# Kernel optimization log

Measured on AMD Instinct MI355X. Metric: run time of the kernel, lower is better.

The kernel has to match this reference:

```python
import jax, jax.numpy as jnp
import numpy as np

B, E, C = 1024, 512, 16384
MRG, ALPHA, V, K, LAM, TAU = 0.1, 32.0, 100.0, 1.0, 0.1, 1.5


def _l2norm(x):
    # matches torch l2_norm: divide by sqrt(sum(x^2) + 1e-12) row-wise
    n = jnp.sqrt(jnp.sum(x * x, axis=1) + 1e-12)
    return x / n[:, None]


def setup_inputs() -> dict:
    key = jax.random.key(0)
    k1, k2, k3, k4, k5 = jax.random.split(key, 5)
    inputsBatch = _l2norm(jax.random.normal(k1, (B, E), dtype=jnp.float32))
    targetsBatch = jax.random.randint(k2, (B,), 0, C, dtype=jnp.int32)
    # kaiming_normal fan_out on (C, E): std = sqrt(2 / E)
    proxies = jax.random.normal(k3, (C, E), dtype=jnp.float32) * np.sqrt(2.0 / E).astype(np.float32)
    effectiveNum = jax.random.uniform(k4, (C,), dtype=jnp.float32) * 100.0
    learnedSim = jax.random.uniform(k5, (C,), dtype=jnp.float32)
    return {"inputsBatch": inputsBatch, "targetsBatch": targetsBatch,
            "proxies": proxies, "effectiveNum": effectiveNum, "learnedSim": learnedSim}


def reference(inputsBatch, targetsBatch, proxies, effectiveNum, learnedSim):
    nb_classes = proxies.shape[0]
    P = jax.nn.one_hot(targetsBatch, nb_classes, dtype=inputsBatch.dtype)  # [B, C]
    N = 1.0 - P
    proxy_l2 = _l2norm(proxies)
    cos = inputsBatch @ proxy_l2.T  # [B, C]

    classCnt = P.sum(axis=0)                      # [C]
    present = (classCnt > 0).astype(cos.dtype)

    w_base = 1.0 / (1.0 + jnp.log1p(effectiveNum))
    eta = (1.0 + K * (1.0 - learnedSim)) * w_base + LAM
    outlierSim = learnedSim - eta                 # [C]

    # enableFilter=False: mask at positive positions stays 1, so each present
    # class contributes mean(ones)=1 to pos_weight_sum
    pos_weight_sum = jnp.sum(present)

    # negative-position adaptive reweighting (vectorized over the class loop)
    neg_vals = jnp.where(cos < outlierSim[None, :],
                         (1.0 / jnp.maximum(1.0, effectiveNum))[None, :],
                         1.0)                      # [B, C]
    Ncnt = N.sum(axis=0)
    neg_mean = jnp.sum(N * neg_vals, axis=0) / jnp.maximum(Ncnt, 1.0)
    neg_weight_sum = jnp.sum(jnp.where(Ncnt > 0, neg_mean, 0.0))

    mask = jnp.where(N > 0, neg_vals, 1.0)        # 1 at positive entries

    pos_term = jnp.sum(jnp.log1p(jnp.sum(P * jnp.exp(ALPHA * (MRG - cos) * mask), axis=0)))
    neg_term = jnp.sum(jnp.log1p(jnp.sum(N * jnp.exp(ALPHA * (cos + MRG) * mask), axis=0)))

    return pos_term / pos_weight_sum + neg_term / neg_weight_sum
```

## Files before the change

### kernel.cpp

```cpp
#include <hip/hip_runtime.h>
#include <math.h>

#define B_SZ 1024
#define E_SZ 512
#define C_SZ 16384
#define MRG 0.1f
#define ALPHA 32.0f
#define K_HY 1.0f
#define LAM 0.1f

typedef __bf16 bf16;
typedef bf16 bf16x8 __attribute__((ext_vector_type(8)));
typedef float f32x4 __attribute__((ext_vector_type(4)));

__device__ __forceinline__ void async16(const void* g, void* l) {
    __builtin_amdgcn_global_load_lds(
        (const __attribute__((address_space(1))) void*)g,
        (__attribute__((address_space(3))) void*)l,
        16, 0, 0);
}

__global__ __launch_bounds__(256) void prep(
    const float* __restrict__ effNum, const float* __restrict__ lSim,
    const float* __restrict__ x,
    float* __restrict__ oSim, float* __restrict__ iEff, bf16* __restrict__ Abf,
    float* __restrict__ posExp, float* __restrict__ negExp,
    float* __restrict__ negVals, int* __restrict__ cCnt,
    float* __restrict__ acc4) {
    int c = blockIdx.x * 256 + threadIdx.x;
    float en = effNum[c], ls = lSim[c];
    float wb = 1.0f / (1.0f + log1pf(en));
    float eta = (1.0f + K_HY * (1.0f - ls)) * wb + LAM;
    oSim[c] = ls - eta;
    iEff[c] = 1.0f / fmaxf(1.0f, en);
    posExp[c] = 0.f; negExp[c] = 0.f; negVals[c] = 0.f; cCnt[c] = 0;
    if (c < 8) acc4[c] = 0.f;
    const float* xp = x + (size_t)c * 32;
    bf16* yp = Abf + (size_t)c * 32;
#pragma unroll
    for (int j = 0; j < 4; ++j) {
        float4 v0 = *(const float4*)(xp + j * 8);
        float4 v1 = *(const float4*)(xp + j * 8 + 4);
        bf16x8 o;
        o[0] = (bf16)v0.x; o[1] = (bf16)v0.y; o[2] = (bf16)v0.z; o[3] = (bf16)v0.w;
        o[4] = (bf16)v1.x; o[5] = (bf16)v1.y; o[6] = (bf16)v1.z; o[7] = (bf16)v1.w;
        *(bf16x8*)(yp + j * 8) = o;
    }
}

__global__ __launch_bounds__(256) void proxy_norm(
    const float* __restrict__ proxies, bf16* __restrict__ Pbf,
    const int* __restrict__ tg, int* __restrict__ cCnt) {
    if (blockIdx.x >= 4096) {
        int i = (blockIdx.x - 4096) * 256 + threadIdx.x;
        atomicAdd(&cCnt[tg[i]], 1);
        return;
    }
    int row = (blockIdx.x * 256 + threadIdx.x) >> 6;
    int lane = threadIdx.x & 63;
    const float* pr = proxies + (size_t)row * E_SZ + lane * 8;
    float4 v0 = *(const float4*)pr;
    float4 v1 = *(const float4*)(pr + 4);
    float ss = v0.x * v0.x + v0.y * v0.y + v0.z * v0.z + v0.w * v0.w +
               v1.x * v1.x + v1.y * v1.y + v1.z * v1.z + v1.w * v1.w;
#pragma unroll
    for (int m = 1; m < 64; m <<= 1) ss += __shfl_xor(ss, m);
    float inv = 1.0f / sqrtf(ss + 1e-12f);
    bf16x8 o;
    o[0] = (bf16)(v0.x * inv); o[1] = (bf16)(v0.y * inv);
    o[2] = (bf16)(v0.z * inv); o[3] = (bf16)(v0.w * inv);
    o[4] = (bf16)(v1.x * inv); o[5] = (bf16)(v1.y * inv);
    o[6] = (bf16)(v1.z * inv); o[7] = (bf16)(v1.w * inv);
    *(bf16x8*)(Pbf + (size_t)row * E_SZ + lane * 8) = o;
}

__global__ __launch_bounds__(256) void gemm_epilogue(
    const bf16* __restrict__ Abf,
    const bf16* __restrict__ Pbf,
    const int* __restrict__ targets,
    const float* __restrict__ oSimA,
    const float* __restrict__ iEffA,
    float* __restrict__ posExp,
    float* __restrict__ negExp,
    float* __restrict__ negVals) {
    __shared__ __align__(16) bf16 Alds[2][128 * 32];
    __shared__ __align__(16) bf16 Blds[2][128 * 32];
    __shared__ int tgtLds[128];

    const int tid = threadIdx.x;
    const int wave = tid >> 6, lane = tid & 63;
    const int quad = lane >> 4, l16 = lane & 15;
    const int wRow = (wave >> 1) * 64, wCol = (wave & 1) * 64;
    const int bn0 = blockIdx.x * 128, bm0 = blockIdx.y * 128;

    if (tid < 128) tgtLds[tid] = targets[bm0 + tid];

    const bf16* gA = Abf + (size_t)(bm0 + wave * 32 + l16) * E_SZ + quad * 8;
    const bf16* gB = Pbf + (size_t)(bn0 + wave * 32 + l16) * E_SZ + quad * 8;

    int colG[4]; float oS[4], iE[4];
#pragma unroll
    for (int ni = 0; ni < 4; ++ni) {
        colG[ni] = bn0 + wCol + ni * 16 + l16;
        oS[ni] = oSimA[colG[ni]];
        iE[ni] = iEffA[colG[ni]];
    }

    f32x4 zero = {0.f, 0.f, 0.f, 0.f};
    f32x4 acc[4][4];
#pragma unroll
    for (int i = 0; i < 4; ++i)
#pragma unroll
        for (int j = 0; j < 4; ++j) acc[i][j] = zero;

#define STAGE(K0, BUF)                                                        \
    {                                                                         \
        _Pragma("unroll")                                                     \
        for (int j = 0; j < 2; ++j) {                                         \
            int chunk = wave * 2 + j;                                         \
            async16(gA + (size_t)j * 16 * E_SZ + (K0), &Alds[BUF][chunk * 512]); \
            async16(gB + (size_t)j * 16 * E_SZ + (K0), &Blds[BUF][chunk * 512]); \
        }                                                                     \
    }

    STAGE(0, 0)
#pragma unroll
    for (int kk = 0; kk < 16; ++kk) {
        __syncthreads();
        if (kk < 15) STAGE((kk + 1) * 32, (kk + 1) & 1)
        const int bsel = kk & 1;
        bf16x8 af[4], bff[4];
#pragma unroll
        for (int mi = 0; mi < 4; ++mi)
            af[mi] = *(const bf16x8*)&Alds[bsel][((wRow >> 4) + mi) * 512 + quad * 128 + l16 * 8];
#pragma unroll
        for (int ni = 0; ni < 4; ++ni)
            bff[ni] = *(const bf16x8*)&Blds[bsel][((wCol >> 4) + ni) * 512 + quad * 128 + l16 * 8];
#pragma unroll
        for (int mi = 0; mi < 4; ++mi)
#pragma unroll
            for (int ni = 0; ni < 4; ++ni)
                acc[mi][ni] = __builtin_amdgcn_mfma_f32_16x16x32_bf16(
                    af[mi], bff[ni], acc[mi][ni], 0, 0, 0);
    }
#undef STAGE

    float negE[4] = {0.f, 0.f, 0.f, 0.f};
    float negV[4] = {0.f, 0.f, 0.f, 0.f};
#pragma unroll
    for (int mi = 0; mi < 4; ++mi) {
#pragma unroll
        for (int r = 0; r < 4; ++r) {
            int rowL = wRow + mi * 16 + quad * 4 + r;
            int tgt = tgtLds[rowL];
#pragma unroll
            for (int ni = 0; ni < 4; ++ni) {
                float cosv = acc[mi][ni][r];
                if (tgt == colG[ni]) {
                    atomicAdd(&posExp[colG[ni]], __expf(ALPHA * (MRG - cosv)));
                } else {
                    float nv = (cosv < oS[ni]) ? iE[ni] : 1.0f;
                    negE[ni] += __expf(ALPHA * (cosv + MRG) * nv);
                    negV[ni] += nv;
                }
            }
        }
    }
#pragma unroll
    for (int ni = 0; ni < 4; ++ni) {
        float e = negE[ni], v = negV[ni];
        e += __shfl_xor(e, 16); e += __shfl_xor(e, 32);
        v += __shfl_xor(v, 16); v += __shfl_xor(v, 32);
        if (quad == 0) {
            atomicAdd(&negExp[colG[ni]], e);
            atomicAdd(&negVals[colG[ni]], v);
        }
    }
}

__global__ __launch_bounds__(256) void finalize_partial(
    const float* __restrict__ posExp, const float* __restrict__ negExp,
    const float* __restrict__ negVals, const int* __restrict__ cCnt,
    float* __restrict__ acc4) {
    int c = blockIdx.x * 256 + threadIdx.x;
    float pt = log1pf(posExp[c]);
    float nt = log1pf(negExp[c]);
    int cnt = cCnt[c];
    float pws = (cnt > 0) ? 1.0f : 0.0f;
    int Nc = B_SZ - cnt;
    float nws = (Nc > 0) ? negVals[c] / (float)Nc : 0.0f;
#pragma unroll
    for (int m = 1; m < 64; m <<= 1) {
        pt += __shfl_xor(pt, m);
        nt += __shfl_xor(nt, m);
        pws += __shfl_xor(pws, m);
        nws += __shfl_xor(nws, m);
    }
    __shared__ float red[4][4];
    int wv = threadIdx.x >> 6;
    if ((threadIdx.x & 63) == 0) {
        red[wv][0] = pt; red[wv][1] = nt; red[wv][2] = pws; red[wv][3] = nws;
    }
    __syncthreads();
    if (threadIdx.x < 4) {
        float s = red[0][threadIdx.x] + red[1][threadIdx.x] +
                  red[2][threadIdx.x] + red[3][threadIdx.x];
        atomicAdd(&acc4[threadIdx.x], s);
    }
}

__global__ void finalize_out(const float* __restrict__ acc4, float* __restrict__ out) {
    out[0] = acc4[0] / acc4[2] + acc4[1] / acc4[3];
}

extern "C" void kernel_launch(void* const* d_in, const int* in_sizes, int n_in,
                              void* d_out, int out_size, void* d_ws, size_t ws_size,
                              hipStream_t stream) {
    const float* inputs = (const float*)d_in[0];
    const int* targets = (const int*)d_in[1];
    const float* proxies = (const float*)d_in[2];
    const float* effNum = (const float*)d_in[3];
    const float* lSim = (const float*)d_in[4];
    float* out = (float*)d_out;

    bf16* Pbf = (bf16*)d_ws;
    bf16* Abf = Pbf + (size_t)C_SZ * E_SZ;
    float* oSim = (float*)(Abf + (size_t)B_SZ * E_SZ);
    float* iEff = oSim + C_SZ;
    float* posExp = iEff + C_SZ;
    float* negExp = posExp + C_SZ;
    float* negVals = negExp + C_SZ;
    int* cCnt = (int*)(negVals + C_SZ);
    float* acc4 = (float*)(cCnt + C_SZ);

    prep<<<C_SZ / 256, 256, 0, stream>>>(effNum, lSim, inputs, oSim, iEff, Abf,
                                         posExp, negExp, negVals, cCnt, acc4);
    proxy_norm<<<4096 + 4, 256, 0, stream>>>(proxies, Pbf, targets, cCnt);
    gemm_epilogue<<<dim3(C_SZ / 128, B_SZ / 128), 256, 0, stream>>>(
        Abf, Pbf, targets, oSim, iEff, posExp, negExp, negVals);
    finalize_partial<<<C_SZ / 256, 256, 0, stream>>>(posExp, negExp, negVals, cCnt, acc4);
    finalize_out<<<1, 1, 0, stream>>>(acc4, out);
}
```

Baseline: 139.6 us.

## Merge prep kernels and load GEMM operands directly from global memory

Merges the prep and proxy_norm kernels into one prologue launch and moves the class-count atomics into the first GEMM block, which removes one kernel launch. The GEMM drops its LDS double-buffered async staging and instead has each wave read its bf16 fragments straight from global memory into registers, with no barriers. Target lookups in the epilogue now read global memory instead of LDS. The cost is that operands are no longer shared through LDS between waves, so there is more global and L2 traffic and no software prefetch overlap.

Result: slower. 159.7 us (+14.4%).

```diff
diff --git a/kernel.cpp b/kernel.cpp
--- a/kernel.cpp
+++ b/kernel.cpp
@@ -13,65 +13,51 @@
 typedef bf16 bf16x8 __attribute__((ext_vector_type(8)));
 typedef float f32x4 __attribute__((ext_vector_type(4)));
 
-__device__ __forceinline__ void async16(const void* g, void* l) {
-    __builtin_amdgcn_global_load_lds(
-        (const __attribute__((address_space(1))) void*)g,
-        (__attribute__((address_space(3))) void*)l,
-        16, 0, 0);
-}
-
-__global__ __launch_bounds__(256) void prep(
+__global__ __launch_bounds__(256) void prologue(
+    const float* __restrict__ proxies, bf16* __restrict__ Pbf,
     const float* __restrict__ effNum, const float* __restrict__ lSim,
-    const float* __restrict__ x,
-    float* __restrict__ oSim, float* __restrict__ iEff, bf16* __restrict__ Abf,
+    const float* __restrict__ x, bf16* __restrict__ Abf,
+    float* __restrict__ oSim, float* __restrict__ iEff,
     float* __restrict__ posExp, float* __restrict__ negExp,
     float* __restrict__ negVals, int* __restrict__ cCnt,
     float* __restrict__ acc4) {
-    int c = blockIdx.x * 256 + threadIdx.x;
-    float en = effNum[c], ls = lSim[c];
-    float wb = 1.0f / (1.0f + log1pf(en));
-    float eta = (1.0f + K_HY * (1.0f - ls)) * wb + LAM;
-    oSim[c] = ls - eta;
-    iEff[c] = 1.0f / fmaxf(1.0f, en);
-    posExp[c] = 0.f; negExp[c] = 0.f; negVals[c] = 0.f; cCnt[c] = 0;
-    if (c < 8) acc4[c] = 0.f;
-    const float* xp = x + (size_t)c * 32;
-    bf16* yp = Abf + (size_t)c * 32;
-#pragma unroll
-    for (int j = 0; j < 4; ++j) {
-        float4 v0 = *(const float4*)(xp + j * 8);
-        float4 v1 = *(const float4*)(xp + j * 8 + 4);
+    if (blockIdx.x < 4096) {
+        int row = (blockIdx.x * 256 + threadIdx.x) >> 6;
+        int lane = threadIdx.x & 63;
+        const float* pr = proxies + (size_t)row * E_SZ + lane * 8;
+        float4 v0 = *(const float4*)pr;
+        float4 v1 = *(const float4*)(pr + 4);
+        float ss = v0.x * v0.x + v0.y * v0.y + v0.z * v0.z + v0.w * v0.w +
+                   v1.x * v1.x + v1.y * v1.y + v1.z * v1.z + v1.w * v1.w;
+#pragma unroll
+        for (int m = 1; m < 64; m <<= 1) ss += __shfl_xor(ss, m);
+        float inv = 1.0f / sqrtf(ss + 1e-12f);
         bf16x8 o;
-        o[0] = (bf16)v0.x; o[1] = (bf16)v0.y; o[2] = (bf16)v0.z; o[3] = (bf16)v0.w;
-        o[4] = (bf16)v1.x; o[5] = (bf16)v1.y; o[6] = (bf16)v1.z; o[7] = (bf16)v1.w;
-        *(bf16x8*)(yp + j * 8) = o;
-    }
-}
-
-__global__ __launch_bounds__(256) void proxy_norm(
-    const float* __restrict__ proxies, bf16* __restrict__ Pbf,
-    const int* __restrict__ tg, int* __restrict__ cCnt) {
-    if (blockIdx.x >= 4096) {
-        int i = (blockIdx.x - 4096) * 256 + threadIdx.x;
-        atomicAdd(&cCnt[tg[i]], 1);
-        return;
-    }
-    int row = (blockIdx.x * 256 + threadIdx.x) >> 6;
-    int lane = threadIdx.x & 63;
-    const float* pr = proxies + (size_t)row * E_SZ + lane * 8;
-    float4 v0 = *(const float4*)pr;
-    float4 v1 = *(const float4*)(pr + 4);
-    float ss = v0.x * v0.x + v0.y * v0.y + v0.z * v0.z + v0.w * v0.w +
-               v1.x * v1.x + v1.y * v1.y + v1.z * v1.z + v1.w * v1.w;
-#pragma unroll
-    for (int m = 1; m < 64; m <<= 1) ss += __shfl_xor(ss, m);
-    float inv = 1.0f / sqrtf(ss + 1e-12f);
-    bf16x8 o;
-    o[0] = (bf16)(v0.x * inv); o[1] = (bf16)(v0.y * inv);
-    o[2] = (bf16)(v0.z * inv); o[3] = (bf16)(v0.w * inv);
-    o[4] = (bf16)(v1.x * inv); o[5] = (bf16)(v1.y * inv);
-    o[6] = (bf16)(v1.z * inv); o[7] = (bf16)(v1.w * inv);
-    *(bf16x8*)(Pbf + (size_t)row * E_SZ + lane * 8) = o;
+        o[0] = (bf16)(v0.x * inv); o[1] = (bf16)(v0.y * inv);
+        o[2] = (bf16)(v0.z * inv); o[3] = (bf16)(v0.w * inv);
+        o[4] = (bf16)(v1.x * inv); o[5] = (bf16)(v1.y * inv);
+        o[6] = (bf16)(v1.z * inv); o[7] = (bf16)(v1.w * inv);
+        *(bf16x8*)(Pbf + (size_t)row * E_SZ + lane * 8) = o;
+    } else {
+        int t = (blockIdx.x - 4096) * 256 + threadIdx.x;
+        float en = effNum[t], ls = lSim[t];
+        float wb = 1.0f / (1.0f + log1pf(en));
+        float eta = (1.0f + K_HY * (1.0f - ls)) * wb + LAM;
+        oSim[t] = ls - eta;
+        iEff[t] = 1.0f / fmaxf(1.0f, en);
+        posExp[t] = 0.f; negExp[t] = 0.f; negVals[t] = 0.f; cCnt[t] = 0;
+        if (t < 8) acc4[t] = 0.f;
+#pragma unroll
+        for (int p = 0; p < 4; ++p) {
+            size_t f0 = ((size_t)p * 16384 + t) * 8;
+            float4 v0 = *(const float4*)(x + f0);
+            float4 v1 = *(const float4*)(x + f0 + 4);
+            bf16x8 o;
+            o[0] = (bf16)v0.x; o[1] = (bf16)v0.y; o[2] = (bf16)v0.z; o[3] = (bf16)v0.w;
+            o[4] = (bf16)v1.x; o[5] = (bf16)v1.y; o[6] = (bf16)v1.z; o[7] = (bf16)v1.w;
+            *(bf16x8*)(Abf + f0) = o;
+        }
+    }
 }
 
 __global__ __launch_bounds__(256) void gemm_epilogue(
@@ -82,21 +68,51 @@
     const float* __restrict__ iEffA,
     float* __restrict__ posExp,
     float* __restrict__ negExp,
-    float* __restrict__ negVals) {
-    __shared__ __align__(16) bf16 Alds[2][128 * 32];
-    __shared__ __align__(16) bf16 Blds[2][128 * 32];
-    __shared__ int tgtLds[128];
-
+    float* __restrict__ negVals,
+    int* __restrict__ cCnt) {
     const int tid = threadIdx.x;
     const int wave = tid >> 6, lane = tid & 63;
     const int quad = lane >> 4, l16 = lane & 15;
     const int wRow = (wave >> 1) * 64, wCol = (wave & 1) * 64;
     const int bn0 = blockIdx.x * 128, bm0 = blockIdx.y * 128;
 
-    if (tid < 128) tgtLds[tid] = targets[bm0 + tid];
-
-    const bf16* gA = Abf + (size_t)(bm0 + wave * 32 + l16) * E_SZ + quad * 8;
-    const bf16* gB = Pbf + (size_t)(bn0 + wave * 32 + l16) * E_SZ + quad * 8;
+    if (blockIdx.x == 0 && blockIdx.y == 0) {
+#pragma unroll
+        for (int j = 0; j < 4; ++j) atomicAdd(&cCnt[targets[j * 256 + tid]], 1);
+    }
+
+    const int aRow = bm0 + wRow + l16;
+    const int bCol = bn0 + wCol + l16;
+    const bf16* aP[4];
+    const bf16* bP[4];
+#pragma unroll
+    for (int mi = 0; mi < 4; ++mi)
+        aP[mi] = Abf + (size_t)(aRow + mi * 16) * E_SZ + quad * 8;
+#pragma unroll
+    for (int ni = 0; ni < 4; ++ni)
+        bP[ni] = Pbf + (size_t)(bCol + ni * 16) * E_SZ + quad * 8;
+
+    f32x4 zero = {0.f, 0.f, 0.f, 0.f};
+    f32x4 acc[4][4];
+#pragma unroll
+    for (int i = 0; i < 4; ++i)
+#pragma unroll
+        for (int j = 0; j < 4; ++j) acc[i][j] = zero;
+
+#pragma unroll
+    for (int k0 = 0; k0 < E_SZ; k0 += 32) {
+        bf16x8 af[4], bff[4];
+#pragma unroll
+        for (int mi = 0; mi < 4; ++mi) af[mi] = *(const bf16x8*)(aP[mi] + k0);
+#pragma unroll
+        for (int ni = 0; ni < 4; ++ni) bff[ni] = *(const bf16x8*)(bP[ni] + k0);
+#pragma unroll
+        for (int mi = 0; mi < 4; ++mi)
+#pragma unroll
+            for (int ni = 0; ni < 4; ++ni)
+                acc[mi][ni] = __builtin_amdgcn_mfma_f32_16x16x32_bf16(
+                    af[mi], bff[ni], acc[mi][ni], 0, 0, 0);
+    }
 
     int colG[4]; float oS[4], iE[4];
 #pragma unroll
@@ -105,54 +121,14 @@
         oS[ni] = oSimA[colG[ni]];
         iE[ni] = iEffA[colG[ni]];
     }
-
-    f32x4 zero = {0.f, 0.f, 0.f, 0.f};
-    f32x4 acc[4][4];
-#pragma unroll
-    for (int i = 0; i < 4; ++i)
-#pragma unroll
-        for (int j = 0; j < 4; ++j) acc[i][j] = zero;
-
-#define STAGE(K0, BUF)                                                        \
-    {                                                                         \
-        _Pragma("unroll")                                                     \
-        for (int j = 0; j < 2; ++j) {                                         \
-            int chunk = wave * 2 + j;                                         \
-            async16(gA + (size_t)j * 16 * E_SZ + (K0), &Alds[BUF][chunk * 512]); \
-            async16(gB + (size_t)j * 16 * E_SZ + (K0), &Blds[BUF][chunk * 512]); \
-        }                                                                     \
-    }
-
-    STAGE(0, 0)
-#pragma unroll
-    for (int kk = 0; kk < 16; ++kk) {
-        __syncthreads();
-        if (kk < 15) STAGE((kk + 1) * 32, (kk + 1) & 1)
-        const int bsel = kk & 1;
-        bf16x8 af[4], bff[4];
-#pragma unroll
-        for (int mi = 0; mi < 4; ++mi)
-            af[mi] = *(const bf16x8*)&Alds[bsel][((wRow >> 4) + mi) * 512 + quad * 128 + l16 * 8];
-#pragma unroll
-        for (int ni = 0; ni < 4; ++ni)
-            bff[ni] = *(const bf16x8*)&Blds[bsel][((wCol >> 4) + ni) * 512 + quad * 128 + l16 * 8];
-#pragma unroll
-        for (int mi = 0; mi < 4; ++mi)
-#pragma unroll
-            for (int ni = 0; ni < 4; ++ni)
-                acc[mi][ni] = __builtin_amdgcn_mfma_f32_16x16x32_bf16(
-                    af[mi], bff[ni], acc[mi][ni], 0, 0, 0);
-    }
-#undef STAGE
-
     float negE[4] = {0.f, 0.f, 0.f, 0.f};
     float negV[4] = {0.f, 0.f, 0.f, 0.f};
 #pragma unroll
     for (int mi = 0; mi < 4; ++mi) {
 #pragma unroll
         for (int r = 0; r < 4; ++r) {
-            int rowL = wRow + mi * 16 + quad * 4 + r;
-            int tgt = tgtLds[rowL];
+            int rowG = bm0 + wRow + mi * 16 + quad * 4 + r;
+            int tgt = targets[rowG];
 #pragma unroll
             for (int ni = 0; ni < 4; ++ni) {
                 float cosv = acc[mi][ni][r];
@@ -233,11 +209,11 @@
     int* cCnt = (int*)(negVals + C_SZ);
     float* acc4 = (float*)(cCnt + C_SZ);
 
-    prep<<<C_SZ / 256, 256, 0, stream>>>(effNum, lSim, inputs, oSim, iEff, Abf,
-                                         posExp, negExp, negVals, cCnt, acc4);
-    proxy_norm<<<4096 + 4, 256, 0, stream>>>(proxies, Pbf, targets, cCnt);
+    prologue<<<4096 + 64, 256, 0, stream>>>(proxies, Pbf, effNum, lSim, inputs,
+                                            Abf, oSim, iEff, posExp, negExp,
+                                            negVals, cCnt, acc4);
     gemm_epilogue<<<dim3(C_SZ / 128, B_SZ / 128), 256, 0, stream>>>(
-        Abf, Pbf, targets, oSim, iEff, posExp, negExp, negVals);
+        Abf, Pbf, targets, oSim, iEff, posExp, negExp, negVals, cCnt);
     finalize_partial<<<C_SZ / 256, 256, 0, stream>>>(posExp, negExp, negVals, cCnt, acc4);
     finalize_out<<<1, 1, 0, stream>>>(acc4, out);
 }
```
